# Kernel tuning notes

Measured on AMD Instinct MI355X. Metric: run time of the kernel, lower is better.

Reference implementation:

```python
import jax, jax.numpy as jnp
import numpy as np

N = 200000      # num entities
D_IN = 256      # input_dim
D_OUT = 256     # output_dim
R = 8           # num_relations
E = 150000      # edges per relation


def _xavier(key, shape):
    fan_in, fan_out = shape[-2], shape[-1]
    bound = (6.0 / (fan_in + fan_out)) ** 0.5
    return jax.random.uniform(key, shape, jnp.float32, -bound, bound)


def setup_inputs() -> dict:
    key = jax.random.key(0)
    ks = jax.random.split(key, 5)
    entity_embeddings = jax.random.normal(ks[0], (N, D_IN), jnp.float32)
    relation_weights = _xavier(ks[1], (R, D_IN, D_OUT))
    self_weight = _xavier(ks[2], (D_IN, D_OUT))
    bias_param = jnp.zeros((R, D_OUT), jnp.float32)
    edge_index = jax.random.randint(ks[3], (R, 2, E), 0, N)  # row0=src, row1=tgt
    edge_weights = jax.random.uniform(ks[4], (R, E), jnp.float32)
    return {
        "entity_embeddings": entity_embeddings,
        "relation_weights": relation_weights,
        "self_weight": self_weight,
        "bias_param": bias_param,
        "edge_index": edge_index,
        "edge_weights": edge_weights,
    }


def reference(entity_embeddings, relation_weights, self_weight, bias_param, edge_index, edge_weights):
    num_entities = entity_embeddings.shape[0]
    d_out = relation_weights.shape[2]

    def per_relation(out, inp):
        ei, ew, W, b = inp
        src, tgt = ei[0], ei[1]
        # gather -> per-relation matmul -> edge-weight scale
        msg = (entity_embeddings[src] @ W) * ew[:, None]          # [E, d_out]
        out = out.at[tgt].add(msg)                                 # scatter-add
        # bias added once per unique target node of this relation
        presence = jnp.zeros((num_entities,), entity_embeddings.dtype).at[tgt].set(1.0)
        out = out + presence[:, None] * b
        return out, None

    out0 = jnp.zeros((num_entities, d_out), entity_embeddings.dtype)
    out, _ = jax.lax.scan(per_relation, out0, (edge_index, edge_weights, relation_weights, bias_param))
    return out + entity_embeddings @ self_weight
```

## Files before the change

kernel.cpp:

```cpp
#include <hip/hip_runtime.h>


#define N_ENT 200000
#define D 256
#define R_REL 8
#define E_EDGE 150000
#define TOT_E (R_REL * E_EDGE)
#define MKEY (N_ENT * R_REL)
#define SCAN_B 1024
#define NBLK_SCAN ((MKEY + SCAN_B - 1) / SCAN_B)

typedef __bf16 bf16x8 __attribute__((ext_vector_type(8)));
typedef unsigned short u16x8 __attribute__((ext_vector_type(8)));
typedef float f32x4 __attribute__((ext_vector_type(4)));

__device__ __forceinline__ unsigned short f2bf(float f) {
  unsigned int u = __builtin_bit_cast(unsigned int, f);
  u += 0x7FFFu + ((u >> 16) & 1u);
  return (unsigned short)(u >> 16);
}
__device__ __forceinline__ float bf2f(unsigned short u) {
  return __builtin_bit_cast(float, ((unsigned)u) << 16);
}
__device__ __forceinline__ f32x4 mfma16(u16x8 a, u16x8 b, f32x4 c) {
  return __builtin_amdgcn_mfma_f32_16x16x32_bf16(
      __builtin_bit_cast(bf16x8, a), __builtin_bit_cast(bf16x8, b), c, 0, 0, 0);
}

__global__ __launch_bounds__(256) void k_cvt_x(const float* __restrict__ x,
                                               unsigned short* __restrict__ xh) {
  int i = blockIdx.x * 256 + threadIdx.x;
  const float4* xv = (const float4*)x;
  float4 a = xv[2 * i], b = xv[2 * i + 1];
  uint4 o;
  o.x = (unsigned)f2bf(a.x) | ((unsigned)f2bf(a.y) << 16);
  o.y = (unsigned)f2bf(a.z) | ((unsigned)f2bf(a.w) << 16);
  o.z = (unsigned)f2bf(b.x) | ((unsigned)f2bf(b.y) << 16);
  o.w = (unsigned)f2bf(b.z) | ((unsigned)f2bf(b.w) << 16);
  ((uint4*)xh)[i] = o;
}

__global__ __launch_bounds__(256) void k_cvt_w(const float* __restrict__ relw,
                                               const float* __restrict__ selfw,
                                               unsigned short* __restrict__ wf) {
  int t = blockIdx.x * 256 + threadIdx.x;
  int rel = t >> 13;
  int rem = t & 8191;
  int kb = rem >> 10;
  int nb = (rem >> 6) & 15;
  int lane = rem & 63;
  const float* W = (rel < R_REL) ? (relw + rel * D * D) : selfw;
  int k0 = kb * 32 + (lane >> 4) * 8;
  int n = nb * 16 + (lane & 15);
  unsigned int o[4];
#pragma unroll
  for (int jj = 0; jj < 4; ++jj) {
    unsigned lo = f2bf(W[(k0 + 2 * jj) * D + n]);
    unsigned hi = f2bf(W[(k0 + 2 * jj + 1) * D + n]);
    o[jj] = lo | (hi << 16);
  }
  ((uint4*)wf)[t] = make_uint4(o[0], o[1], o[2], o[3]);
}

__global__ __launch_bounds__(256) void k_cvt_bias(const float* __restrict__ bias,
                                                  unsigned short* __restrict__ bb) {
  int t = blockIdx.x * 256 + threadIdx.x;
  int nb = t >> 6, lane = t & 63;
  int lk = lane >> 4, n = nb * 16 + (lane & 15);
  unsigned int o[4];
#pragma unroll
  for (int jj = 0; jj < 4; ++jj) {
    unsigned lo = 0, hi = 0;
    if (lk == 0) {
      lo = f2bf(bias[(2 * jj) * D + n]);
      hi = f2bf(bias[(2 * jj + 1) * D + n]);
    }
    o[jj] = lo | (hi << 16);
  }
  ((uint4*)bb)[t] = make_uint4(o[0], o[1], o[2], o[3]);
}

__global__ __launch_bounds__(256) void k_hist(const int* __restrict__ ei,
                                              unsigned* __restrict__ counts) {
  int t = blockIdx.x * 256 + threadIdx.x;
  if (t >= TOT_E) return;
  int r = t / E_EDGE, e = t - r * E_EDGE;
  int tgt = ei[(r * 2 + 1) * E_EDGE + e];
  atomicAdd(&counts[r * N_ENT + tgt], 1u);
}

__global__ __launch_bounds__(256) void k_scan1(const unsigned* __restrict__ cnt,
                                               unsigned* __restrict__ off,
                                               unsigned* __restrict__ aux) {
  __shared__ unsigned sc[256];
  int tid = threadIdx.x;
  int base = blockIdx.x * SCAN_B + tid * 4;
  unsigned v[4];
#pragma unroll
  for (int j = 0; j < 4; ++j) v[j] = (base + j < MKEY) ? cnt[base + j] : 0u;
  unsigned s = v[0] + v[1] + v[2] + v[3];
  sc[tid] = s;
  __syncthreads();
  for (int o = 1; o < 256; o <<= 1) {
    unsigned t = (tid >= o) ? sc[tid - o] : 0u;
    __syncthreads();
    sc[tid] += t;
    __syncthreads();
  }
  unsigned excl = sc[tid] - s;
  if (tid == 255) aux[blockIdx.x] = sc[255];
#pragma unroll
  for (int j = 0; j < 4; ++j) {
    if (base + j < MKEY) off[base + j] = excl;
    excl += v[j];
  }
}

__global__ __launch_bounds__(256) void k_scan2(unsigned* __restrict__ aux) {
  __shared__ unsigned sc[256];
  int tid = threadIdx.x;
  int base = tid * 7;
  unsigned v[7];
#pragma unroll
  for (int j = 0; j < 7; ++j) v[j] = (base + j < NBLK_SCAN) ? aux[base + j] : 0u;
  unsigned s = 0;
#pragma unroll
  for (int j = 0; j < 7; ++j) s += v[j];
  sc[tid] = s;
  __syncthreads();
  for (int o = 1; o < 256; o <<= 1) {
    unsigned t = (tid >= o) ? sc[tid - o] : 0u;
    __syncthreads();
    sc[tid] += t;
    __syncthreads();
  }
  unsigned excl = sc[tid] - s;
#pragma unroll
  for (int j = 0; j < 7; ++j) {
    if (base + j < NBLK_SCAN) aux[base + j] = excl;
    excl += v[j];
  }
}

__global__ __launch_bounds__(256) void k_scan3(unsigned* __restrict__ off,
                                               const unsigned* __restrict__ aux) {
  unsigned add = aux[blockIdx.x];
  int base = blockIdx.x * SCAN_B + threadIdx.x * 4;
  if (base + 3 < MKEY) {
    uint4* p = (uint4*)(off + base);
    uint4 x = *p;
    x.x += add; x.y += add; x.z += add; x.w += add;
    *p = x;
  } else {
    for (int j = 0; j < 4; ++j)
      if (base + j < MKEY) off[base + j] += add;
  }
}

__global__ __launch_bounds__(256) void k_scatter(const int* __restrict__ ei,
                                                 const float* __restrict__ ew,
                                                 unsigned* __restrict__ off,
                                                 unsigned* __restrict__ spack,
                                                 float* __restrict__ sewt) {
  int t = blockIdx.x * 256 + threadIdx.x;
  if (t >= TOT_E) return;
  int r = t / E_EDGE, e = t - r * E_EDGE;
  int tgt = ei[(r * 2 + 1) * E_EDGE + e];
  int src = ei[(r * 2) * E_EDGE + e];
  float w = ew[t];
  unsigned pos = atomicAdd(&off[r * N_ENT + tgt], 1u);
  spack[pos] = (unsigned)src | ((unsigned)(tgt & 63) << 18);
  sewt[pos] = w;
}

__global__ __launch_bounds__(512, 2) void k_main(const unsigned short* __restrict__ xh,
                                                 const unsigned short* __restrict__ wf,
                                                 const unsigned short* __restrict__ bbf,
                                                 const unsigned* __restrict__ counts,
                                                 const unsigned* __restrict__ off_end,
                                                 const unsigned* __restrict__ spack,
                                                 const float* __restrict__ sewt,
                                                 float* __restrict__ out) {
  __shared__ __align__(16) unsigned char As[64 * 512];
  int n0 = blockIdx.x * 64;
  int tid = threadIdx.x;
  int w = tid >> 6, lane = tid & 63;
  int lm = lane & 15, lk = lane >> 4;
  int rbase = (w >> 2) * 32;
  int cbase = (w & 3) * 4;

  unsigned sB[8], eE[8];
#pragma unroll
  for (int r = 0; r < 8; ++r) {
    int kb2 = r * N_ENT + n0 + w * 8;
    sB[r] = kb2 ? off_end[kb2 - 1] : 0u;
    eE[r] = off_end[kb2 + 7];
  }
  unsigned pk0[8];
  float wt0[8];
#pragma unroll
  for (int r = 0; r < 8; ++r) {
    unsigned idx = sB[r] + (unsigned)lane;
    if (idx >= (unsigned)TOT_E) idx = (unsigned)(TOT_E - 1);
    pk0[r] = spack[idx];
    wt0[r] = sewt[idx];
  }

  f32x4 acc[2][4] = {};

  {
    const unsigned short* wfb = wf + 8 * 65536;
#pragma unroll
    for (int kb = 0; kb < 8; ++kb) {
      u16x8 a[2], b[4];
#pragma unroll
      for (int mi = 0; mi < 2; ++mi)
        a[mi] = *(const u16x8*)(xh + (size_t)(n0 + rbase + mi * 16 + lm) * 256 + kb * 32 + lk * 8);
#pragma unroll
      for (int ni = 0; ni < 4; ++ni)
        b[ni] = *(const u16x8*)(wfb + ((kb * 16 + cbase + ni) * 64 + lane) * 8);
#pragma unroll
      for (int mi = 0; mi < 2; ++mi)
#pragma unroll
        for (int ni = 0; ni < 4; ++ni)
          acc[mi][ni] = mfma16(a[mi], b[ni], acc[mi][ni]);
    }
  }

#pragma unroll
  for (int r = 0; r < 8; ++r) {
#pragma unroll
    for (int k = 0; k < 8; ++k) {
      int g = w * 8 + k;
      int wb = (g * 512 + lane * 8) ^ ((g & 7) << 4);
      *(uint2*)(As + wb) = make_uint2(0u, 0u);
    }

    unsigned s0 = sB[r], e0 = eE[r];
    int gp = -1;
    float a0 = 0.f, a1 = 0.f, a2 = 0.f, a3 = 0.f;
    unsigned pkv = pk0[r];
    float wtv = wt0[r];
    for (unsigned chunk = s0; chunk < e0; chunk += 64u) {
      if (chunk != s0) {
        unsigned idx = chunk + (unsigned)lane;
        if (idx >= (unsigned)TOT_E) idx = (unsigned)(TOT_E - 1);
        pkv = spack[idx];
        wtv = sewt[idx];
      }
      unsigned rem = e0 - chunk;
      int m = rem < 64u ? (int)rem : 64;
      for (int g8 = 0; g8 < m; g8 += 8) {
        unsigned pk8[8];
        float wt8[8];
#pragma unroll
        for (int u = 0; u < 8; ++u) {
          pk8[u] = (unsigned)__shfl((int)pkv, g8 + u);
          wt8[u] = __shfl(wtv, g8 + u);
        }
        ushort4 xv[8];
#pragma unroll
        for (int u = 0; u < 8; ++u) {
          unsigned srcu = (g8 + u < m) ? (pk8[u] & 0x3FFFFu) : 0u;
          xv[u] = *(const ushort4*)(xh + (size_t)srcu * 256 + lane * 4);
        }
#pragma unroll
        for (int u = 0; u < 8; ++u) {
          if (g8 + u < m) {
            int g = (int)(pk8[u] >> 18);
            if (g != gp) {
              if (gp >= 0) {
                unsigned lo = (unsigned)f2bf(a0) | ((unsigned)f2bf(a1) << 16);
                unsigned hi = (unsigned)f2bf(a2) | ((unsigned)f2bf(a3) << 16);
                int wb = (gp * 512 + lane * 8) ^ ((gp & 7) << 4);
                *(uint2*)(As + wb) = make_uint2(lo, hi);
              }
              a0 = a1 = a2 = a3 = 0.f;
              gp = g;
            }
            float wt = wt8[u];
            a0 += wt * bf2f(xv[u].x);
            a1 += wt * bf2f(xv[u].y);
            a2 += wt * bf2f(xv[u].z);
            a3 += wt * bf2f(xv[u].w);
          }
        }
      }
    }
    if (gp >= 0) {
      unsigned lo = (unsigned)f2bf(a0) | ((unsigned)f2bf(a1) << 16);
      unsigned hi = (unsigned)f2bf(a2) | ((unsigned)f2bf(a3) << 16);
      int wb = (gp * 512 + lane * 8) ^ ((gp & 7) << 4);
      *(uint2*)(As + wb) = make_uint2(lo, hi);
    }
    __syncthreads();

    const unsigned short* wfb = wf + r * 65536;
#pragma unroll
    for (int kb = 0; kb < 8; ++kb) {
      u16x8 a[2], b[4];
#pragma unroll
      for (int mi = 0; mi < 2; ++mi) {
        int row = rbase + mi * 16 + lm;
        int byt = (row * 512 + kb * 64 + lk * 16) ^ ((row & 7) << 4);
        a[mi] = *(const u16x8*)(As + byt);
      }
#pragma unroll
      for (int ni = 0; ni < 4; ++ni)
        b[ni] = *(const u16x8*)(wfb + ((kb * 16 + cbase + ni) * 64 + lane) * 8);
#pragma unroll
      for (int mi = 0; mi < 2; ++mi)
#pragma unroll
        for (int ni = 0; ni < 4; ++ni)
          acc[mi][ni] = mfma16(a[mi], b[ni], acc[mi][ni]);
    }
    __syncthreads();
  }

  {
    u16x8 bb[4];
#pragma unroll
    for (int ni = 0; ni < 4; ++ni)
      bb[ni] = *(const u16x8*)(bbf + ((cbase + ni) * 64 + lane) * 8);
#pragma unroll
    for (int mi = 0; mi < 2; ++mi) {
      u16x8 pa = {};
      if (lk == 0) {
        int n = n0 + rbase + mi * 16 + lm;
#pragma unroll
        for (int r = 0; r < 8; ++r)
          pa[r] = counts[r * N_ENT + n] ? 0x3F80 : 0;
      }
#pragma unroll
      for (int ni = 0; ni < 4; ++ni)
        acc[mi][ni] = mfma16(pa, bb[ni], acc[mi][ni]);
    }
  }

#pragma unroll
  for (int mi = 0; mi < 2; ++mi)
#pragma unroll
    for (int ni = 0; ni < 4; ++ni) {
      int col = (w & 3) * 64 + ni * 16 + lm;
#pragma unroll
      for (int j = 0; j < 4; ++j) {
        int row = n0 + rbase + mi * 16 + lk * 4 + j;
        out[row * 256 + col] = acc[mi][ni][j];
      }
    }
}

extern "C" void kernel_launch(void* const* d_in, const int* in_sizes, int n_in,
                              void* d_out, int out_size, void* d_ws, size_t ws_size,
                              hipStream_t stream) {
  const float* x = (const float*)d_in[0];
  const float* relw = (const float*)d_in[1];
  const float* selfw = (const float*)d_in[2];
  const float* bias = (const float*)d_in[3];
  const int* ei = (const int*)d_in[4];
  const float* ew = (const float*)d_in[5];
  float* out = (float*)d_out;

  char* ws = (char*)d_ws;
  unsigned short* xh = (unsigned short*)ws;
  unsigned short* wf = (unsigned short*)(ws + 102400000);
  unsigned short* bbf = (unsigned short*)(ws + 103579648);
  unsigned* counts = (unsigned*)(ws + 103596032);
  unsigned* offs = (unsigned*)(ws + 109996032);
  unsigned* aux = (unsigned*)(ws + 116396032);
  unsigned* spack = (unsigned*)(ws + 116404224);
  float* sewt = (float*)(ws + 121204224);

  hipMemsetAsync(counts, 0, (size_t)MKEY * 4, stream);
  k_cvt_x<<<(N_ENT * D) / 2048, 256, 0, stream>>>(x, xh);
  k_cvt_w<<<288, 256, 0, stream>>>(relw, selfw, wf);
  k_cvt_bias<<<4, 256, 0, stream>>>(bias, bbf);
  k_hist<<<(TOT_E + 255) / 256, 256, 0, stream>>>(ei, counts);
  k_scan1<<<NBLK_SCAN, 256, 0, stream>>>(counts, offs, aux);
  k_scan2<<<1, 256, 0, stream>>>(aux);
  k_scan3<<<NBLK_SCAN, 256, 0, stream>>>(offs, aux);
  k_scatter<<<(TOT_E + 255) / 256, 256, 0, stream>>>(ei, ew, offs, spack, sewt);
  k_main<<<N_ENT / 64, 512, 0, stream>>>(xh, wf, bbf, counts, offs, spack, sewt, out);
}
```

Baseline: 789.0 us.

## Double-buffer aggregated tile to overlap next relation's gather with current MFMA

Doubles the shared-memory aggregation buffer so the block can zero the buffer and issue the first batch of gather loads for relation r+1 before running the MFMA pass for relation r. It finishes that aggregation after the MFMAs, which removes one barrier per relation. The self-weight matmul is moved ahead of the edge prefetch. The goal is to hide gather latency behind matrix math. In exchange, LDS use grows to 64KB per block and register pressure rises, which may reduce occupancy under launch_bounds(512,2).

```diff
diff --git a/kernel.cpp b/kernel.cpp
--- a/kernel.cpp
+++ b/kernel.cpp
@@ -173,6 +173,141 @@
   sewt[pos] = w;
 }
 
+__device__ __forceinline__ void agg_issue(int g0, int lane, unsigned s0, unsigned e0,
+                                          unsigned pkc, float wtc,
+                                          const unsigned short* __restrict__ xh,
+                                          unsigned char* nxt,
+                                          unsigned pk8[8], float wt8[8], ushort4 xv[8]) {
+#pragma unroll
+  for (int k = 0; k < 8; ++k) {
+    int g = g0 + k;
+    int wb = (g * 512 + lane * 8) ^ ((g & 7) << 4);
+    *(uint2*)(nxt + wb) = make_uint2(0u, 0u);
+  }
+  int total = (int)(e0 - s0);
+  int m0 = total < 8 ? total : 8;
+#pragma unroll
+  for (int u = 0; u < 8; ++u) {
+    pk8[u] = (unsigned)__shfl((int)pkc, u);
+    wt8[u] = __shfl(wtc, u);
+  }
+#pragma unroll
+  for (int u = 0; u < 8; ++u) {
+    unsigned srcu = (u < m0) ? (pk8[u] & 0x3FFFFu) : 0u;
+    xv[u] = *(const ushort4*)(xh + (size_t)srcu * 256 + lane * 4);
+  }
+}
+
+__device__ __forceinline__ void agg_finish(int lane, unsigned s0, unsigned e0,
+                                           unsigned pkc, float wtc,
+                                           const unsigned* __restrict__ spack,
+                                           const float* __restrict__ sewt,
+                                           const unsigned short* __restrict__ xh,
+                                           unsigned char* nxt,
+                                           const unsigned pk8[8], const float wt8[8],
+                                           const ushort4 xv[8]) {
+  int total = (int)(e0 - s0);
+  if (total <= 0) return;
+  int gp = -1;
+  float a0 = 0.f, a1 = 0.f, a2 = 0.f, a3 = 0.f;
+#define AGG_FLUSH() do { \
+    unsigned lo_ = (unsigned)f2bf(a0) | ((unsigned)f2bf(a1) << 16); \
+    unsigned hi_ = (unsigned)f2bf(a2) | ((unsigned)f2bf(a3) << 16); \
+    int wb_ = (gp * 512 + lane * 8) ^ ((gp & 7) << 4); \
+    *(uint2*)(nxt + wb_) = make_uint2(lo_, hi_); } while (0)
+
+  int mch = total < 64 ? total : 64;
+  int m0 = mch < 8 ? mch : 8;
+#pragma unroll
+  for (int u = 0; u < 8; ++u) {
+    if (u < m0) {
+      int g = (int)(pk8[u] >> 18);
+      if (g != gp) {
+        if (gp >= 0) AGG_FLUSH();
+        a0 = a1 = a2 = a3 = 0.f;
+        gp = g;
+      }
+      float wt = wt8[u];
+      a0 += wt * bf2f(xv[u].x);
+      a1 += wt * bf2f(xv[u].y);
+      a2 += wt * bf2f(xv[u].z);
+      a3 += wt * bf2f(xv[u].w);
+    }
+  }
+  for (int g8 = 8; g8 < mch; g8 += 8) {
+    unsigned q8[8];
+    float v8[8];
+#pragma unroll
+    for (int u = 0; u < 8; ++u) {
+      q8[u] = (unsigned)__shfl((int)pkc, g8 + u);
+      v8[u] = __shfl(wtc, g8 + u);
+    }
+    ushort4 yv[8];
+#pragma unroll
+    for (int u = 0; u < 8; ++u) {
+      unsigned srcu = (g8 + u < mch) ? (q8[u] & 0x3FFFFu) : 0u;
+      yv[u] = *(const ushort4*)(xh + (size_t)srcu * 256 + lane * 4);
+    }
+#pragma unroll
+    for (int u = 0; u < 8; ++u) {
+      if (g8 + u < mch) {
+        int g = (int)(q8[u] >> 18);
+        if (g != gp) {
+          if (gp >= 0) AGG_FLUSH();
+          a0 = a1 = a2 = a3 = 0.f;
+          gp = g;
+        }
+        float wt = v8[u];
+        a0 += wt * bf2f(yv[u].x);
+        a1 += wt * bf2f(yv[u].y);
+        a2 += wt * bf2f(yv[u].z);
+        a3 += wt * bf2f(yv[u].w);
+      }
+    }
+  }
+  for (unsigned chunk = s0 + 64u; chunk < e0; chunk += 64u) {
+    unsigned idx = chunk + (unsigned)lane;
+    if (idx >= (unsigned)TOT_E) idx = (unsigned)(TOT_E - 1);
+    unsigned pkv = spack[idx];
+    float wtv = sewt[idx];
+    int rem = (int)(e0 - chunk);
+    int m = rem < 64 ? rem : 64;
+    for (int g8 = 0; g8 < m; g8 += 8) {
+      unsigned q8[8];
+      float v8[8];
+#pragma unroll
+      for (int u = 0; u < 8; ++u) {
+        q8[u] = (unsigned)__shfl((int)pkv, g8 + u);
+        v8[u] = __shfl(wtv, g8 + u);
+      }
+      ushort4 yv[8];
+#pragma unroll
+      for (int u = 0; u < 8; ++u) {
+        unsigned srcu = (g8 + u < m) ? (q8[u] & 0x3FFFFu) : 0u;
+        yv[u] = *(const ushort4*)(xh + (size_t)srcu * 256 + lane * 4);
+      }
+#pragma unroll
+      for (int u = 0; u < 8; ++u) {
+        if (g8 + u < m) {
+          int g = (int)(q8[u] >> 18);
+          if (g != gp) {
+            if (gp >= 0) AGG_FLUSH();
+            a0 = a1 = a2 = a3 = 0.f;
+            gp = g;
+          }
+          float wt = v8[u];
+          a0 += wt * bf2f(yv[u].x);
+          a1 += wt * bf2f(yv[u].y);
+          a2 += wt * bf2f(yv[u].z);
+          a3 += wt * bf2f(yv[u].w);
+        }
+      }
+    }
+  }
+  if (gp >= 0) AGG_FLUSH();
+#undef AGG_FLUSH
+}
+
 __global__ __launch_bounds__(512, 2) void k_main(const unsigned short* __restrict__ xh,
                                                  const unsigned short* __restrict__ wf,
                                                  const unsigned short* __restrict__ bbf,
@@ -181,13 +316,14 @@
                                                  const unsigned* __restrict__ spack,
                                                  const float* __restrict__ sewt,
                                                  float* __restrict__ out) {
-  __shared__ __align__(16) unsigned char As[64 * 512];
+  __shared__ __align__(16) unsigned char As[2 * 32768];
   int n0 = blockIdx.x * 64;
   int tid = threadIdx.x;
   int w = tid >> 6, lane = tid & 63;
   int lm = lane & 15, lk = lane >> 4;
   int rbase = (w >> 2) * 32;
   int cbase = (w & 3) * 4;
+  int g0 = w * 8;
 
   unsigned sB[8], eE[8];
 #pragma unroll
@@ -196,6 +332,28 @@
     sB[r] = kb2 ? off_end[kb2 - 1] : 0u;
     eE[r] = off_end[kb2 + 7];
   }
+
+  f32x4 acc[2][4] = {};
+
+  {
+    const unsigned short* wfb = wf + 8 * 65536;
+#pragma unroll
+    for (int kb = 0; kb < 8; ++kb) {
+      u16x8 a[2], b[4];
+#pragma unroll
+      for (int mi = 0; mi < 2; ++mi)
+        a[mi] = *(const u16x8*)(xh + (size_t)(n0 + rbase + mi * 16 + lm) * 256 + kb * 32 + lk * 8);
+#pragma unroll
+      for (int ni = 0; ni < 4; ++ni)
+        b[ni] = *(const u16x8*)(wfb + ((kb * 16 + cbase + ni) * 64 + lane) * 8);
+#pragma unroll
+      for (int mi = 0; mi < 2; ++mi)
+#pragma unroll
+        for (int ni = 0; ni < 4; ++ni)
+          acc[mi][ni] = mfma16(a[mi], b[ni], acc[mi][ni]);
+    }
+  }
+
   unsigned pk0[8];
   float wt0[8];
 #pragma unroll
@@ -206,94 +364,24 @@
     wt0[r] = sewt[idx];
   }
 
-  f32x4 acc[2][4] = {};
-
   {
-    const unsigned short* wfb = wf + 8 * 65536;
-#pragma unroll
-    for (int kb = 0; kb < 8; ++kb) {
-      u16x8 a[2], b[4];
-#pragma unroll
-      for (int mi = 0; mi < 2; ++mi)
-        a[mi] = *(const u16x8*)(xh + (size_t)(n0 + rbase + mi * 16 + lm) * 256 + kb * 32 + lk * 8);
-#pragma unroll
-      for (int ni = 0; ni < 4; ++ni)
-        b[ni] = *(const u16x8*)(wfb + ((kb * 16 + cbase + ni) * 64 + lane) * 8);
-#pragma unroll
-      for (int mi = 0; mi < 2; ++mi)
-#pragma unroll
-        for (int ni = 0; ni < 4; ++ni)
-          acc[mi][ni] = mfma16(a[mi], b[ni], acc[mi][ni]);
-    }
-  }
+    unsigned pk8[8];
+    float wt8[8];
+    ushort4 xv[8];
+    agg_issue(g0, lane, sB[0], eE[0], pk0[0], wt0[0], xh, As, pk8, wt8, xv);
+    agg_finish(lane, sB[0], eE[0], pk0[0], wt0[0], spack, sewt, xh, As, pk8, wt8, xv);
+  }
+  __syncthreads();
 
 #pragma unroll
   for (int r = 0; r < 8; ++r) {
-#pragma unroll
-    for (int k = 0; k < 8; ++k) {
-      int g = w * 8 + k;
-      int wb = (g * 512 + lane * 8) ^ ((g & 7) << 4);
-      *(uint2*)(As + wb) = make_uint2(0u, 0u);
-    }
-
-    unsigned s0 = sB[r], e0 = eE[r];
-    int gp = -1;
-    float a0 = 0.f, a1 = 0.f, a2 = 0.f, a3 = 0.f;
-    unsigned pkv = pk0[r];
-    float wtv = wt0[r];
-    for (unsigned chunk = s0; chunk < e0; chunk += 64u) {
-      if (chunk != s0) {
-        unsigned idx = chunk + (unsigned)lane;
-        if (idx >= (unsigned)TOT_E) idx = (unsigned)(TOT_E - 1);
-        pkv = spack[idx];
-        wtv = sewt[idx];
-      }
-      unsigned rem = e0 - chunk;
-      int m = rem < 64u ? (int)rem : 64;
-      for (int g8 = 0; g8 < m; g8 += 8) {
-        unsigned pk8[8];
-        float wt8[8];
-#pragma unroll
-        for (int u = 0; u < 8; ++u) {
-          pk8[u] = (unsigned)__shfl((int)pkv, g8 + u);
-          wt8[u] = __shfl(wtv, g8 + u);
-        }
-        ushort4 xv[8];
-#pragma unroll
-        for (int u = 0; u < 8; ++u) {
-          unsigned srcu = (g8 + u < m) ? (pk8[u] & 0x3FFFFu) : 0u;
-          xv[u] = *(const ushort4*)(xh + (size_t)srcu * 256 + lane * 4);
-        }
-#pragma unroll
-        for (int u = 0; u < 8; ++u) {
-          if (g8 + u < m) {
-            int g = (int)(pk8[u] >> 18);
-            if (g != gp) {
-              if (gp >= 0) {
-                unsigned lo = (unsigned)f2bf(a0) | ((unsigned)f2bf(a1) << 16);
-                unsigned hi = (unsigned)f2bf(a2) | ((unsigned)f2bf(a3) << 16);
-                int wb = (gp * 512 + lane * 8) ^ ((gp & 7) << 4);
-                *(uint2*)(As + wb) = make_uint2(lo, hi);
-              }
-              a0 = a1 = a2 = a3 = 0.f;
-              gp = g;
-            }
-            float wt = wt8[u];
-            a0 += wt * bf2f(xv[u].x);
-            a1 += wt * bf2f(xv[u].y);
-            a2 += wt * bf2f(xv[u].z);
-            a3 += wt * bf2f(xv[u].w);
-          }
-        }
-      }
-    }
-    if (gp >= 0) {
-      unsigned lo = (unsigned)f2bf(a0) | ((unsigned)f2bf(a1) << 16);
-      unsigned hi = (unsigned)f2bf(a2) | ((unsigned)f2bf(a3) << 16);
-      int wb = (gp * 512 + lane * 8) ^ ((gp & 7) << 4);
-      *(uint2*)(As + wb) = make_uint2(lo, hi);
-    }
-    __syncthreads();
+    unsigned char* cur = As + (r & 1) * 32768;
+    unsigned char* nxt = As + ((r + 1) & 1) * 32768;
+    unsigned pk8[8];
+    float wt8[8];
+    ushort4 xv[8];
+    if (r < 7)
+      agg_issue(g0, lane, sB[r + 1], eE[r + 1], pk0[r + 1], wt0[r + 1], xh, nxt, pk8, wt8, xv);
 
     const unsigned short* wfb = wf + r * 65536;
 #pragma unroll
@@ -303,7 +391,7 @@
       for (int mi = 0; mi < 2; ++mi) {
         int row = rbase + mi * 16 + lm;
         int byt = (row * 512 + kb * 64 + lk * 16) ^ ((row & 7) << 4);
-        a[mi] = *(const u16x8*)(As + byt);
+        a[mi] = *(const u16x8*)(cur + byt);
       }
 #pragma unroll
       for (int ni = 0; ni < 4; ++ni)
@@ -314,6 +402,10 @@
         for (int ni = 0; ni < 4; ++ni)
           acc[mi][ni] = mfma16(a[mi], b[ni], acc[mi][ni]);
     }
+
+    if (r < 7)
+      agg_finish(lane, sB[r + 1], eE[r + 1], pk0[r + 1], wt0[r + 1], spack, sewt, xh, nxt,
+                 pk8, wt8, xv);
     __syncthreads();
   }
 
```

New measurement: 754.9 us. 1.05x faster.
